# Performance work log

Measured on AMD Instinct MI355X. Metric: run time of the kernel, lower is better.

## Reference

```python
import jax, jax.numpy as jnp
import numpy as np

NUM_REC = 22
P = 24            # nodes per graph
G = 8192          # graphs in batch
N = G * P         # 196608 nodes
E = N * 4         # 786432 edges (avg degree 4)
F_NODE = 96       # 74 chem features + 22 receptor one-hot
F_EDGE = 16
EPS = 1e-5
NEG_SLOPE = 0.2   # GATv2 default negative_slope


def gatv2(x, src, dst, edge_attr, Wl, bl, Wr, br, We, att, bo):
    """PyG GATv2Conv (heads=1, add_self_loops=True, fill_value='mean'), eval mode."""
    n = x.shape[0]
    # self loops with edge_attr = mean of incoming edge attrs per target node
    deg = jax.ops.segment_sum(jnp.ones_like(dst, dtype=x.dtype), dst, num_segments=n)
    loop_attr = jax.ops.segment_sum(edge_attr, dst, num_segments=n) / jnp.maximum(deg, 1.0)[:, None]
    loop = jnp.arange(n, dtype=src.dtype)
    s = jnp.concatenate([src, loop])           # [E+N] source
    d = jnp.concatenate([dst, loop])           # [E+N] target
    ea = jnp.concatenate([edge_attr, loop_attr], axis=0)
    xl = x @ Wl + bl                           # source transform [n, C]
    xr = x @ Wr + br                           # target transform [n, C]
    m = xl[s] + xr[d] + ea @ We                # [E+N, C]
    e = jax.nn.leaky_relu(m, NEG_SLOPE) @ att  # [E+N] attention logits
    # segment softmax over target nodes (every node has its self loop -> no empty segment)
    emax = jax.ops.segment_max(e, d, num_segments=n)
    ez = jnp.exp(e - emax[d])
    denom = jax.ops.segment_sum(ez, d, num_segments=n)
    alpha = ez / denom[d]
    return jax.ops.segment_sum(alpha[:, None] * xl[s], d, num_segments=n) + bo


def batchnorm(h, gamma, beta):
    # training-style BN (batch statistics, biased var) as in torch BatchNorm1d forward
    mu = h.mean(0)
    var = h.var(0)
    return gamma * (h - mu) * jax.lax.rsqrt(var + EPS) + beta


def setup_inputs() -> dict:
    key = jax.random.key(0)
    ks = jax.random.split(key, 40)
    x = jax.random.normal(ks[0], (N, F_NODE), jnp.float32)
    # intra-graph, self-loop-free edges
    src = jax.random.randint(ks[1], (E,), 0, N)
    off = jax.random.randint(ks[2], (E,), 1, P)
    dst = (src // P) * P + (src % P + off) % P
    edge_index = jnp.stack([src, dst]).astype(jnp.int32)
    edge_attr = jax.random.normal(ks[3], (E, F_EDGE), jnp.float32)
    batch = (jnp.arange(N) // P).astype(jnp.int32)

    def lin(k, i, o):
        return jax.random.normal(k, (i, o), jnp.float32) * 0.1

    def vec(k, o):
        return jax.random.normal(k, (o,), jnp.float32) * 0.1

    Fin = F_NODE - NUM_REC  # 74
    return {
        "x": x, "edge_index": edge_index, "edge_attr": edge_attr, "batch": batch,
        # GATv2 layer 1 (74 -> 32)
        "Wl1": lin(ks[4], Fin, 32), "bl1": vec(ks[5], 32),
        "Wr1": lin(ks[6], Fin, 32), "br1": vec(ks[7], 32),
        "We1": lin(ks[8], F_EDGE, 32), "att1": vec(ks[9], 32), "bo1": vec(ks[10], 32),
        # GATv2 layer 2 (32 -> 8)
        "Wl2": lin(ks[11], 32, 8), "bl2": vec(ks[12], 8),
        "Wr2": lin(ks[13], 32, 8), "br2": vec(ks[14], 8),
        "We2": lin(ks[15], F_EDGE, 8), "att2": vec(ks[16], 8), "bo2": vec(ks[17], 8),
        # BatchNorm affine
        "g1": jnp.ones((32,), jnp.float32), "be1": jnp.zeros((32,), jnp.float32),
        "g2": jnp.ones((8,), jnp.float32), "be2": jnp.zeros((8,), jnp.float32),
        # MLP head (8+22=30 -> 32 -> 16 -> 8 -> 4 -> 2)
        "fc1_W": lin(ks[18], 8 + NUM_REC, 32), "fc1_b": vec(ks[19], 32),
        "fc2_W": lin(ks[20], 32, 16), "fc2_b": vec(ks[21], 16),
        "fc3_W": lin(ks[22], 16, 8), "fc3_b": vec(ks[23], 8),
        "fc4_W": lin(ks[24], 8, 4), "fc4_b": vec(ks[25], 4),
        "out_W": lin(ks[26], 4, 2), "out_b": vec(ks[27], 2),
    }


def reference(x, edge_index, edge_attr, batch,
              Wl1, bl1, Wr1, br1, We1, att1, bo1,
              Wl2, bl2, Wr2, br2, We2, att2, bo2,
              g1, be1, g2, be2,
              fc1_W, fc1_b, fc2_W, fc2_b, fc3_W, fc3_b, fc4_W, fc4_b, out_W, out_b):
    src, dst = edge_index[0], edge_index[1]
    # per-graph receptor features = last NUM_REC cols of the first node of each graph
    first_idx = jnp.searchsorted(batch, jnp.arange(G, dtype=batch.dtype))
    rec_feat = x[first_idx, -NUM_REC:]                       # [G, 22]
    xin = x[:, :-NUM_REC]                                    # [N, 74]

    h = jax.nn.relu(gatv2(xin, src, dst, edge_attr, Wl1, bl1, Wr1, br1, We1, att1, bo1))
    h = batchnorm(h, g1, be1)                                # [N, 32]
    h = jax.nn.sigmoid(gatv2(h, src, dst, edge_attr, Wl2, bl2, Wr2, br2, We2, att2, bo2))
    h = batchnorm(h, g2, be2)                                # [N, 8]

    cnt = jax.ops.segment_sum(jnp.ones((x.shape[0], 1), x.dtype), batch, num_segments=G)
    pooled = jax.ops.segment_sum(h, batch, num_segments=G) / cnt  # global_mean_pool [G, 8]

    z = jnp.concatenate([pooled, rec_feat], axis=1)          # [G, 30]
    z = jax.nn.relu(z @ fc1_W + fc1_b)
    z = jax.nn.relu(z @ fc2_W + fc2_b)
    z = jax.nn.relu(z @ fc3_W + fc3_b)
    z = jax.nn.relu(z @ fc4_W + fc4_b)
    return z @ out_W + out_b                                 # [G, 2]
```

## Files before the change

### kernel.cpp

```cpp
#include <hip/hip_runtime.h>

typedef unsigned short u16;
typedef unsigned int   u32;
typedef __attribute__((ext_vector_type(4))) float f4_t;
typedef __attribute__((ext_vector_type(4))) unsigned short us4_t;

#define GG 8192
#define PP 24
#define NN 196608
#define EE 786432
#define CAP 176

#define oWl1 0
#define oWr1 2368
#define obl1 4736
#define obr1 4768
#define oWe1 4800
#define oatt1 5312
#define obo1 5344
#define oWl2 5376
#define oWr2 5632
#define obl2 5888
#define obr2 5896
#define oWe2 5904
#define oatt2 6032
#define obo2 6040
#define ofc1W 6048
#define ofc1b 7008
#define ofc2W 7040
#define ofc2b 7552
#define ofc3W 7568
#define ofc3b 7696
#define ofc4W 7704
#define ofc4b 7736
#define ooutW 7740
#define ooutb 7748

#define oW1I 0
#define oW2P 4864
#define oB2P 5376

__device__ __forceinline__ float bf2f(u16 u){
  union { u32 i; float f; } x; x.i = ((u32)u) << 16; return x.f;
}
__device__ __forceinline__ u32 fkey(float f){
  int i = __float_as_int(f);
  return (i >= 0) ? (((u32)i) | 0x80000000u) : ~((u32)i);
}
__device__ __forceinline__ float funkey(u32 k){
  u32 i = (k & 0x80000000u) ? (k & 0x7FFFFFFFu) : ~k;
  return __uint_as_float(i);
}
__device__ __forceinline__ float lrelu(float m){ return m > 0.f ? m : 0.2f*m; }
__device__ __forceinline__ float sexp(float a){ return __expf(fminf(a, 0.f)); }
__device__ __forceinline__ float ldf(const void* p, size_t i, int isf){
  return isf ? ((const float*)p)[i] : bf2f(((const u16*)p)[i]);
}

__global__ void k_zero(float* __restrict__ out){
  int i = blockIdx.x*256 + threadIdx.x;
  if(i < GG*2) out[i] = 0.f;
}

__global__ void k_count(const int* __restrict__ dst, int* __restrict__ cnt){
  int e = blockIdx.x*256 + threadIdx.x;
  if(e < EE){
    u32 d = (u32)dst[e];
    if(d < (u32)NN) atomicAdd(&cnt[d], 1);
  }
}

__global__ void k_scanA(const int* __restrict__ cnt, int* __restrict__ offs,
                        int* __restrict__ bsum){
  __shared__ int part[1024];
  int t = threadIdx.x;
  int i = blockIdx.x*1024 + t;
  int c = cnt[i];
  part[t] = c; __syncthreads();
  for(int off=1; off<1024; off<<=1){
    int v = (t>=off) ? part[t-off] : 0;
    __syncthreads();
    part[t] += v;
    __syncthreads();
  }
  offs[i] = part[t] - c;
  if(t==1023) bsum[blockIdx.x] = part[1023];
}

__global__ void k_scanB(int* __restrict__ bsum, int* __restrict__ offs){
  __shared__ int part[256];
  int t = threadIdx.x;
  int c = (t < 192) ? bsum[t] : 0;
  part[t] = c; __syncthreads();
  for(int off=1; off<256; off<<=1){
    int v = (t>=off) ? part[t-off] : 0;
    __syncthreads();
    part[t] += v;
    __syncthreads();
  }
  if(t < 192) bsum[t] = part[t] - c;
  if(t == 255) offs[NN] = part[255];
}

__global__ void k_scanC(int* __restrict__ offs, const int* __restrict__ bsum,
                        int* __restrict__ cursor){
  int t = threadIdx.x;
  int i = blockIdx.x*1024 + t;
  int v = offs[i] + bsum[blockIdx.x];
  offs[i] = v;
  cursor[i] = v;
}

__global__ void k_scatter(const int* __restrict__ src, const int* __restrict__ dst,
                          int* __restrict__ cursor, int* __restrict__ spack){
  int e = blockIdx.x*256 + threadIdx.x;
  if(e < EE){
    u32 d = (u32)dst[e];
    if(d >= (u32)NN) return;
    int g = d / PP;
    int pos = atomicAdd(&cursor[d], 1);
    if((u32)pos < (u32)EE){
      int sl = src[e] - g*PP;
      if((u32)sl > 23u) sl = 0;
      spack[pos] = sl | ((int)(d - g*PP) << 5) | (e << 10);
    }
  }
}

__global__ void k_eaperm(const int* __restrict__ spack, const int* __restrict__ offs,
                         const void* __restrict__ ea, const int* __restrict__ dflag,
                         float* __restrict__ eap){
  int i = blockIdx.x*256 + threadIdx.x;
  if(i >= EE) return;
  if(i >= offs[NN]) return;
  int isf = dflag[0];
  u32 id = ((u32)spack[i]) >> 10;
  if(id >= (u32)EE) id = 0;
  float* o = eap + (size_t)i*16;
  if(isf){
    const float* er = (const float*)ea + (size_t)id*16;
    #pragma unroll
    for(int q=0;q<4;q++) *(f4_t*)(o + q*4) = *(const f4_t*)(er + q*4);
  } else {
    const u16* er = (const u16*)ea + (size_t)id*16;
    #pragma unroll
    for(int c=0;c<16;c++) o[c] = bf2f(er[c]);
  }
}

__global__ void k_wconv(float* __restrict__ wb, float* __restrict__ wq, int* __restrict__ dflag,
    const u32* __restrict__ xw,
    const void* Wl1, const void* bl1, const void* Wr1, const void* br1,
    const void* We1, const void* att1, const void* bo1,
    const void* Wl2, const void* bl2, const void* Wr2, const void* br2,
    const void* We2, const void* att2, const void* bo2,
    const void* f1W, const void* f1b, const void* f2W, const void* f2b,
    const void* f3W, const void* f3b, const void* f4W, const void* f4b,
    const void* oW,  const void* ob)
{
  __shared__ u32 mx[256];
  int t = threadIdx.x;
  u32 m = 0;
  for(int i=t; i<2048; i+=256){
    u32 e = (xw[i] >> 7) & 0xFFu;
    m = m > e ? m : e;
  }
  mx[t] = m; __syncthreads();
  for(int off=128; off>0; off>>=1){
    if(t<off) mx[t] = mx[t] > mx[t+off] ? mx[t] : mx[t+off];
    __syncthreads();
  }
  int isf = (mx[0] > 140u) ? 1 : 0;
  if(t==0) dflag[0] = isf;
  #define CP(off,src,len) for(int i=t;i<(len);i+=256) wb[(off)+i]=ldf(src,i,isf);
  CP(oWl1,Wl1,2368) CP(oWr1,Wr1,2368) CP(obl1,bl1,32) CP(obr1,br1,32)
  CP(oWe1,We1,512)  CP(oatt1,att1,32) CP(obo1,bo1,32)
  CP(oWl2,Wl2,256)  CP(oWr2,Wr2,256)  CP(obl2,bl2,8)  CP(obr2,br2,8)
  CP(oWe2,We2,128)  CP(oatt2,att2,8)  CP(obo2,bo2,8)
  CP(ofc1W,f1W,960) CP(ofc1b,f1b,32)  CP(ofc2W,f2W,512) CP(ofc2b,f2b,16)
  CP(ofc3W,f3W,128) CP(ofc3b,f3b,8)   CP(ofc4W,f4W,32)  CP(ofc4b,f4b,4)
  CP(ooutW,oW,8)    CP(ooutb,ob,2)
  #undef CP
  for(int i=t; i<76*64; i+=256){
    int k = i>>6, cc = i&63, mat = cc>>5, c = cc&31;
    wq[oW1I + i] = (k < 74) ? ldf(mat ? Wr1 : Wl1, k*32 + c, isf) : 0.f;
  }
}

__global__ void k_prep2(float* __restrict__ wq, const float* __restrict__ wb,
                        const float* __restrict__ stats1){
  int t = threadIdx.x;
  for(int i=t; i<512; i+=256){
    int k = i>>4, cc = i&15, mat = cc>>3, c = cc&7;
    wq[oW2P + i] = stats1[k] * wb[(mat ? oWr2 : oWl2) + k*8 + c];
  }
  if(t < 16){
    int mat = t>>3, c = t&7;
    float s = wb[(mat ? obr2 : obl2) + c];
    for(int k=0;k<32;k++) s += stats1[32+k] * wb[(mat ? oWr2 : oWl2) + k*8 + c];
    wq[oB2P + t] = s;
  }
}

__global__ __launch_bounds__(256, 6) void k_l1stats(
    const void* __restrict__ x, const void* __restrict__ ea, const float* __restrict__ eap,
    const float* __restrict__ wb, const float* __restrict__ wq,
    const int* __restrict__ offs, const int* __restrict__ spack, const int* __restrict__ dflag,
    float* __restrict__ p1sum, float* __restrict__ p1sq,
    float* __restrict__ h1, int use_h1)
{
  __shared__ __align__(16) float sEaF[CAP][16];
  __shared__ __align__(16) float sXl[24][36];
  __shared__ float sXr[24][33];
  __shared__ float sEaSum[24][17];
  __shared__ float sEv[CAP];
  __shared__ int   sSl[CAP];
  __shared__ int   sRO[25];
  __shared__ float sSelfE[24];
  __shared__ float sPS[4][32], sPQ[4][32];

  const int t = threadIdx.x;
  const int g = blockIdx.x;
  const int wid = t >> 6;
  const int lane = t & 63;
  const int isf = dflag[0];
  const int nb = g*PP;
  const int eb = offs[nb];
  int ecnt = offs[nb+24] - eb; if(ecnt < 0) ecnt = 0; if(ecnt > CAP) ecnt = CAP;

  if(t < 25){
    int v = offs[nb+t] - eb;
    if(v < 0) v = 0; if(v > CAP) v = CAP;
    sRO[t] = v;
  }
  if(eap){
    for(int i=t; i<ecnt; i+=256) sSl[i] = spack[eb+i] & 1023;
    for(int i=t; i<ecnt*4; i+=256){
      int e = i>>2, q = i&3;
      *(f4_t*)&sEaF[e][q*4] = *(const f4_t*)(eap + ((size_t)(eb+e))*16 + q*4);
    }
  } else {
    for(int i=t; i<ecnt; i+=256){
      int sp = spack[eb+i];
      sSl[i] = sp & 1023;
      u32 id = ((u32)sp) >> 10;
      if(id >= (u32)EE) id = 0;
      if(isf){
        const float* er = (const float*)ea + (size_t)id*16;
        #pragma unroll
        for(int q=0;q<4;q++) *(f4_t*)&sEaF[i][q*4] = *(const f4_t*)(er + q*4);
      } else {
        #pragma unroll
        for(int c=0;c<16;c++) sEaF[i][c] = bf2f(((const u16*)ea)[(size_t)id*16 + c]);
      }
    }
  }
  {
    int rz = wid*6;
    for(int i=lane; i<6*17; i+=64) sEaSum[rz + i/17][i%17] = 0.f;
  }

  {
    const int c = t & 31, mat = (t>>5)&1, w = wid, cc = t&63;
    const float* gW = wq + oW1I;
    float bi = wb[(mat ? obr1 : obl1) + c];
    float acc[6];
    #pragma unroll
    for(int j=0;j<6;j++) acc[j] = bi;
    if(isf){
      const float* xr0 = (const float*)x + (size_t)(nb + w*6)*96;
      for(int kb=0; kb<19; kb++){
        float w0 = gW[(kb*4+0)*64 + cc];
        float w1 = gW[(kb*4+1)*64 + cc];
        float w2 = gW[(kb*4+2)*64 + cc];
        float w3 = gW[(kb*4+3)*64 + cc];
        #pragma unroll
        for(int j=0;j<6;j++){
          f4_t xv = *(const f4_t*)(xr0 + (size_t)j*96 + kb*4);
          acc[j] += xv[0]*w0 + xv[1]*w1 + xv[2]*w2 + xv[3]*w3;
        }
      }
    } else {
      const u16* xr0 = (const u16*)x + (size_t)(nb + w*6)*96;
      for(int kb=0; kb<19; kb++){
        float w0 = gW[(kb*4+0)*64 + cc];
        float w1 = gW[(kb*4+1)*64 + cc];
        float w2 = gW[(kb*4+2)*64 + cc];
        float w3 = gW[(kb*4+3)*64 + cc];
        #pragma unroll
        for(int j=0;j<6;j++){
          us4_t xv = *(const us4_t*)(xr0 + (size_t)j*96 + kb*4);
          acc[j] += bf2f(xv[0])*w0 + bf2f(xv[1])*w1 + bf2f(xv[2])*w2 + bf2f(xv[3])*w3;
        }
      }
    }
    if(mat){
      #pragma unroll
      for(int j=0;j<6;j++) sXr[w*6+j][c] = acc[j];
    } else {
      #pragma unroll
      for(int j=0;j<6;j++) sXl[w*6+j][c] = acc[j];
    }
  }
  __syncthreads();

  const int r0 = wid*6;
  const int a0 = sRO[r0], a1 = sRO[r0+6];
  const int c = t & 31, eo = (t>>5)&1;

  float wr[16];
  #pragma unroll
  for(int k=0;k<16;k++) wr[k] = wb[oWe1 + k*32 + c];
  const float av = wb[oatt1 + c];
  const float bv = wb[obo1 + c];

  for(int base=a0; base<a1; base+=2){
    int e = base + eo;
    bool valid = (e < a1);
    int ec = valid ? e : a0;
    int sp = sSl[ec];
    int sl = sp & 31; if(sl > 23) sl = 0;
    int dl = (sp >> 5) & 31; if(dl > 23) dl = 0;
    f4_t A0 = *(const f4_t*)&sEaF[ec][0];
    f4_t A1 = *(const f4_t*)&sEaF[ec][4];
    f4_t A2 = *(const f4_t*)&sEaF[ec][8];
    f4_t A3 = *(const f4_t*)&sEaF[ec][12];
    float p = A0[0]*wr[0]+A0[1]*wr[1]+A0[2]*wr[2]+A0[3]*wr[3]
            + A1[0]*wr[4]+A1[1]*wr[5]+A1[2]*wr[6]+A1[3]*wr[7]
            + A2[0]*wr[8]+A2[1]*wr[9]+A2[2]*wr[10]+A2[3]*wr[11]
            + A3[0]*wr[12]+A3[1]*wr[13]+A3[2]*wr[14]+A3[3]*wr[15];
    if(valid && c < 16) atomicAdd(&sEaSum[dl][c], sEaF[ec][c]);
    float v = lrelu(sXl[sl][c] + sXr[dl][c] + p) * av;
    v += __shfl_xor(v, 16);
    v += __shfl_xor(v, 8);
    v += __shfl_xor(v, 4);
    v += __shfl_xor(v, 2);
    v += __shfl_xor(v, 1);
    if(valid && c == 0) sEv[e] = v;
  }

  #pragma unroll
  for(int rp=0; rp<3; rp++){
    int r = r0 + rp*2 + eo;
    int deg = sRO[r+1] - sRO[r];
    float invd = 1.f / (float)(deg > 0 ? deg : 1);
    float mp = 0.f;
    #pragma unroll
    for(int k=0;k<16;k++) mp += sEaSum[r][k] * wr[k];
    float v = lrelu(sXl[r][c] + sXr[r][c] + mp*invd) * av;
    v += __shfl_xor(v, 16);
    v += __shfl_xor(v, 8);
    v += __shfl_xor(v, 4);
    v += __shfl_xor(v, 2);
    v += __shfl_xor(v, 1);
    if(c == 0) sSelfE[r] = v;
  }

  float ps = 0.f, pq = 0.f;
  const int h = (t >> 5) & 1;
  #pragma unroll
  for(int j=0;j<6;j++){
    int r = r0 + j;
    int a = sRO[r], b = sRO[r+1];
    float selfE = sSelfE[r];
    float mx = -3.4e38f;
    for(int e=a+lane; e<b; e+=64) mx = fmaxf(mx, sEv[e]);
    mx = fmaxf(mx, __shfl_xor(mx, 32));
    mx = fmaxf(mx, __shfl_xor(mx, 16));
    mx = fmaxf(mx, __shfl_xor(mx, 8));
    mx = fmaxf(mx, __shfl_xor(mx, 4));
    mx = fmaxf(mx, __shfl_xor(mx, 2));
    mx = fmaxf(mx, __shfl_xor(mx, 1));
    float m = fmaxf(mx, selfE);
    float ds = 0.f;
    for(int e=a+lane; e<b; e+=64){
      float z = sexp(sEv[e] - m);
      sEv[e] = z;
      ds += z;
    }
    ds += __shfl_xor(ds, 32);
    ds += __shfl_xor(ds, 16);
    ds += __shfl_xor(ds, 8);
    ds += __shfl_xor(ds, 4);
    ds += __shfl_xor(ds, 2);
    ds += __shfl_xor(ds, 1);
    float selfZ = sexp(selfE - m);
    float rden = 1.f / fmaxf(ds + selfZ, 1e-30f);
    float acc = 0.f;
    for(int e=a+h; e<b; e+=2){
      int sl = sSl[e] & 31; if(sl > 23) sl = 0;
      acc += sEv[e] * sXl[sl][c];
    }
    acc += __shfl_xor(acc, 32);
    float out = (acc + selfZ * sXl[r][c]) * rden;
    out = fmaxf(out + bv, 0.f);
    if(h == 0){
      if(use_h1) h1[((size_t)nb + r)*32 + c] = out;
      ps += out; pq += out*out;
    }
  }
  if(h == 0){ sPS[wid][c] = ps; sPQ[wid][c] = pq; }
  __syncthreads();
  if(t < 32){
    p1sum[g*32+t] = sPS[0][t]+sPS[1][t]+sPS[2][t]+sPS[3][t];
    p1sq[g*32+t]  = sPQ[0][t]+sPQ[1][t]+sPQ[2][t]+sPQ[3][t];
  }
}

__global__ void k_reduce(const float* __restrict__ ps, const float* __restrict__ pq,
                         const void* __restrict__ gamma, const void* __restrict__ beta,
                         const int* __restrict__ dflag,
                         float* __restrict__ stats, int F){
  __shared__ float rs[256], rq[256];
  int f = blockIdx.x, t = threadIdx.x;
  float s=0.f, q=0.f;
  for(int g=t; g<GG; g+=256){ s += ps[g*F+f]; q += pq[g*F+f]; }
  rs[t]=s; rq[t]=q; __syncthreads();
  for(int off=128; off>0; off>>=1){
    if(t<off){ rs[t]+=rs[t+off]; rq[t]+=rq[t+off]; }
    __syncthreads();
  }
  if(t==0){
    int isf = dflag[0];
    float mu  = rs[0] * (1.f/(float)NN);
    float var = rq[0] * (1.f/(float)NN) - mu*mu;
    if(var < 0.f) var = 0.f;
    float sc  = ldf(gamma,f,isf) / sqrtf(var + 1e-5f);
    stats[f]   = sc;
    stats[F+f] = ldf(beta,f,isf) - mu*sc;
  }
}

__global__ __launch_bounds__(256, 6) void k_fused2_h1(
    const void* __restrict__ ea, const float* __restrict__ eap,
    const float* __restrict__ wb, const float* __restrict__ wq,
    const float* __restrict__ h1,
    const int* __restrict__ offs, const int* __restrict__ spack, const int* __restrict__ dflag,
    float* __restrict__ gsum2, float* __restrict__ gsq2)
{
  __shared__ __align__(16) float sEaF[CAP][16];
  __shared__ float sXl2[24][12], sXr2[24][12];
  __shared__ float sEaSum[24][17];
  __shared__ float sEv[CAP];
  __shared__ int   sSl[CAP];
  __shared__ int   sRO[25];
  __shared__ float sSelfE[24];
  __shared__ float sGS[4][8], sGQ[4][8];

  const int t = threadIdx.x;
  const int g = blockIdx.x;
  const int wid = t >> 6;
  const int lane = t & 63;
  const int isf = dflag[0];
  const int nb = g*PP;
  const int eb = offs[nb];
  int ecnt = offs[nb+24] - eb; if(ecnt < 0) ecnt = 0; if(ecnt > CAP) ecnt = CAP;

  if(t < 25){
    int v = offs[nb+t] - eb;
    if(v < 0) v = 0; if(v > CAP) v = CAP;
    sRO[t] = v;
  }
  if(eap){
    for(int i=t; i<ecnt; i+=256) sSl[i] = spack[eb+i] & 1023;
    for(int i=t; i<ecnt*4; i+=256){
      int e = i>>2, q = i&3;
      *(f4_t*)&sEaF[e][q*4] = *(const f4_t*)(eap + ((size_t)(eb+e))*16 + q*4);
    }
  } else {
    for(int i=t; i<ecnt; i+=256){
      int sp = spack[eb+i];
      sSl[i] = sp & 1023;
      u32 id = ((u32)sp) >> 10;
      if(id >= (u32)EE) id = 0;
      if(isf){
        const float* er = (const float*)ea + (size_t)id*16;
        #pragma unroll
        for(int q=0;q<4;q++) *(f4_t*)&sEaF[i][q*4] = *(const f4_t*)(er + q*4);
      } else {
        #pragma unroll
        for(int c=0;c<16;c++) sEaF[i][c] = bf2f(((const u16*)ea)[(size_t)id*16 + c]);
      }
    }
  }
  {
    int rz = wid*6;
    for(int i=lane; i<6*17; i+=64) sEaSum[rz + i/17][i%17] = 0.f;
    for(int i=lane; i<96; i+=64){
      int rl = i>>4, cc = i&15;
      int r = rz + rl;
      float s = wq[oB2P + cc];
      const float* hr = h1 + ((size_t)nb + r)*32;
      #pragma unroll
      for(int q=0;q<8;q++){
        f4_t hv = *(const f4_t*)(hr + q*4);
        s += hv[0]*wq[oW2P+(q*4+0)*16+cc] + hv[1]*wq[oW2P+(q*4+1)*16+cc]
           + hv[2]*wq[oW2P+(q*4+2)*16+cc] + hv[3]*wq[oW2P+(q*4+3)*16+cc];
      }
      if(cc < 8) sXl2[r][cc] = s; else sXr2[r][cc-8] = s;
    }
  }
  __syncthreads();

  const int r0 = wid*6;
  const int a0 = sRO[r0], a1 = sRO[r0+6];
  const int c = t & 7;
  const int eo = lane >> 3;

  float wr[16];
  #pragma unroll
  for(int k=0;k<16;k++) wr[k] = wb[oWe2 + k*8 + c];
  const float av = wb[oatt2 + c];
  const float bv = wb[obo2 + c];

  for(int base=a0; base<a1; base+=8){
    int e = base + eo;
    bool valid = (e < a1);
    int ec = valid ? e : a0;
    int sp = sSl[ec];
    int sl = sp & 31; if(sl > 23) sl = 0;
    int dl = (sp >> 5) & 31; if(dl > 23) dl = 0;
    f4_t A0 = *(const f4_t*)&sEaF[ec][0];
    f4_t A1 = *(const f4_t*)&sEaF[ec][4];
    f4_t A2 = *(const f4_t*)&sEaF[ec][8];
    f4_t A3 = *(const f4_t*)&sEaF[ec][12];
    float p = A0[0]*wr[0]+A0[1]*wr[1]+A0[2]*wr[2]+A0[3]*wr[3]
            + A1[0]*wr[4]+A1[1]*wr[5]+A1[2]*wr[6]+A1[3]*wr[7]
            + A2[0]*wr[8]+A2[1]*wr[9]+A2[2]*wr[10]+A2[3]*wr[11]
            + A3[0]*wr[12]+A3[1]*wr[13]+A3[2]*wr[14]+A3[3]*wr[15];
    if(valid){
      atomicAdd(&sEaSum[dl][c],   sEaF[ec][c]);
      atomicAdd(&sEaSum[dl][c+8], sEaF[ec][c+8]);
    }
    float v = lrelu(sXl2[sl][c] + sXr2[dl][c] + p) * av;
    v += __shfl_xor(v, 4);
    v += __shfl_xor(v, 2);
    v += __shfl_xor(v, 1);
    if(valid && c == 0) sEv[e] = v;
  }

  {
    int rr = r0 + (eo < 6 ? eo : 0);
    bool valid = (eo < 6);
    int deg = sRO[rr+1] - sRO[rr];
    float invd = 1.f / (float)(deg > 0 ? deg : 1);
    float mp = 0.f;
    #pragma unroll
    for(int k=0;k<16;k++) mp += sEaSum[rr][k] * wr[k];
    float v = lrelu(sXl2[rr][c] + sXr2[rr][c] + mp*invd) * av;
    v += __shfl_xor(v, 4);
    v += __shfl_xor(v, 2);
    v += __shfl_xor(v, 1);
    if(valid && c == 0) sSelfE[rr] = v;
  }

  float gs = 0.f, gq = 0.f;
  #pragma unroll
  for(int j=0;j<6;j++){
    int r = r0 + j;
    int a = sRO[r], b = sRO[r+1];
    float selfE = sSelfE[r];
    float mx = -3.4e38f;
    for(int e=a+lane; e<b; e+=64) mx = fmaxf(mx, sEv[e]);
    mx = fmaxf(mx, __shfl_xor(mx, 32));
    mx = fmaxf(mx, __shfl_xor(mx, 16));
    mx = fmaxf(mx, __shfl_xor(mx, 8));
    mx = fmaxf(mx, __shfl_xor(mx, 4));
    mx = fmaxf(mx, __shfl_xor(mx, 2));
    mx = fmaxf(mx, __shfl_xor(mx, 1));
    float m = fmaxf(mx, selfE);
    float ds = 0.f;
    for(int e=a+lane; e<b; e+=64){
      float z = sexp(sEv[e] - m);
      sEv[e] = z;
      ds += z;
    }
    ds += __shfl_xor(ds, 32);
    ds += __shfl_xor(ds, 16);
    ds += __shfl_xor(ds, 8);
    ds += __shfl_xor(ds, 4);
    ds += __shfl_xor(ds, 2);
    ds += __shfl_xor(ds, 1);
    float selfZ = sexp(selfE - m);
    float rden = 1.f / fmaxf(ds + selfZ, 1e-30f);
    float acc = 0.f;
    for(int e=a+eo; e<b; e+=8){
      int sl = sSl[e] & 31; if(sl > 23) sl = 0;
      acc += sEv[e] * sXl2[sl][c];
    }
    acc += __shfl_xor(acc, 8);
    acc += __shfl_xor(acc, 16);
    acc += __shfl_xor(acc, 32);
    float out = (acc + selfZ * sXl2[r][c]) * rden;
    float s = 1.f / (1.f + __expf(-(out + bv)));
    if(eo == 0){ gs += s; gq += s*s; }
  }
  if(eo == 0){ sGS[wid][c] = gs; sGQ[wid][c] = gq; }
  __syncthreads();
  if(t < 8){
    gsum2[g*8+t] = sGS[0][t]+sGS[1][t]+sGS[2][t]+sGS[3][t];
    gsq2[g*8+t]  = sGQ[0][t]+sGQ[1][t]+sGQ[2][t]+sGQ[3][t];
  }
}

__global__ __launch_bounds__(256) void k_fused2_rec(
    const void* __restrict__ x, const void* __restrict__ ea,
    const float* __restrict__ wb, const float* __restrict__ stats1,
    const int* __restrict__ offs, const int* __restrict__ spack, const int* __restrict__ dflag,
    float* __restrict__ gsum2, float* __restrict__ gsq2)
{
  __shared__ float sXrow[24][76];
  __shared__ float sEaF[CAP][17];
  __shared__ __align__(16) float sXl[24][36];
  __shared__ __align__(16) float sXr[24][36];
  __shared__ __align__(16) float sOut[24][36];
  __shared__ float sH[24][33];
  __shared__ float sXl2[24][12], sXr2[24][12], sOut2[24][12];
  __shared__ float sEapSum[24][32];
  __shared__ float sEv[CAP], sEz[CAP];
  __shared__ int   sSp[CAP];
  __shared__ int   sDeg[24];
  __shared__ u32   sMaxU[24];
  __shared__ float sMaxF[24], sDen[24], sSelfZ[24];
  __shared__ float sAtt[32], sBo[32], sSc[32], sSh[32];

  const int t = threadIdx.x;
  const int g = blockIdx.x;
  const int isf = dflag[0];
  int eb = offs[g*24], ee = offs[(g+1)*24];
  if(eb < 0) eb = 0; if(eb > EE) eb = EE;
  if(ee < eb) ee = eb; if(ee > EE) ee = EE;
  int ecnt = ee - eb; if(ecnt > CAP) ecnt = CAP;

  for(int i=t; i<24*74; i+=256){
    int r = i/74, c = i%74;
    sXrow[r][c] = ldf(x, (size_t)(g*PP + r)*96 + c, isf);
  }
  for(int i=t; i<CAP; i+=256) sSp[i] = (i<ecnt) ? spack[eb+i] : 0;
  if(t < 32){ sAtt[t]=wb[oatt1+t]; sBo[t]=wb[obo1+t]; sSc[t]=stats1[t]; sSh[t]=stats1[32+t]; }
  if(t < 24){ sDeg[t]=0; sMaxU[t]=0u; sDen[t]=0.f; }
  for(int i=t; i<24*32; i+=256) sEapSum[i>>5][i&31] = 0.f;
  __syncthreads();
  for(int i=t; i<CAP*16; i+=256){
    int e = i>>4, c = i&15;
    float v = 0.f;
    if(e < ecnt){
      u32 id = ((u32)sSp[e]) >> 10;
      if(id >= (u32)EE) id = 0;
      v = ldf(ea, (size_t)id*16 + c, isf);
    }
    sEaF[e][c] = v;
  }
  __syncthreads();

  {
    int c = t & 31, rr0 = t >> 5;
    for(int r = rr0; r < 24; r += 8){
      float al = wb[obl1+c], ar = wb[obr1+c];
      for(int k=0;k<74;k++){
        float xv = sXrow[r][k];
        al += xv * wb[oWl1 + k*32 + c];
        ar += xv * wb[oWr1 + k*32 + c];
      }
      sXl[r][c] = al; sXr[r][c] = ar;
    }
  }
  __syncthreads();

  for(int e=t; e<ecnt; e+=256){
    int sp = sSp[e];
    int sl = sp & 31; if(sl > 23) sl = 0;
    int dl = (sp >> 5) & 31; if(dl > 23) dl = 0;
    float ev = 0.f;
    for(int c=0;c<32;c++){
      float p = 0.f;
      for(int k=0;k<16;k++) p += sEaF[e][k] * wb[oWe1 + k*32 + c];
      atomicAdd(&sEapSum[dl][c], p);
      ev += lrelu(sXl[sl][c] + sXr[dl][c] + p) * sAtt[c];
    }
    sEv[e] = ev;
    atomicMax(&sMaxU[dl], fkey(ev));
    atomicAdd(&sDeg[dl], 1);
  }
  __syncthreads();

  if(t < 24){
    float invd = 1.f / (float)(sDeg[t] > 0 ? sDeg[t] : 1);
    float ev = 0.f;
    for(int c=0;c<32;c++)
      ev += lrelu(sXl[t][c] + sXr[t][c] + sEapSum[t][c]*invd) * sAtt[c];
    float mxv = (sDeg[t] > 0) ? fmaxf(funkey(sMaxU[t]), ev) : ev;
    sMaxF[t] = mxv;
    float z = sexp(ev - mxv);
    sSelfZ[t] = z;
    sDen[t] = z;
  }
  __syncthreads();

  for(int e=t; e<ecnt; e+=256){
    int dl = (sSp[e]>>5)&31; if(dl > 23) dl = 0;
    float z = sexp(sEv[e] - sMaxF[dl]);
    sEz[e] = z;
    atomicAdd(&sDen[dl], z);
  }
  __syncthreads();

  for(int e=t; e<ecnt; e+=256){
    int dl = (sSp[e]>>5)&31; if(dl > 23) dl = 0;
    sEz[e] /= fmaxf(sDen[dl], 1e-30f);
  }
  if(t < 24) sSelfZ[t] /= fmaxf(sDen[t], 1e-30f);
  __syncthreads();

  for(int o=t; o<24*8; o+=256){
    int nl = o >> 3, cq = (o & 7)*4;
    float al = sSelfZ[nl];
    f4_t xv = *(const f4_t*)&sXl[nl][cq];
    f4_t r;
    #pragma unroll
    for(int j=0;j<4;j++) r[j] = al*xv[j];
    *(f4_t*)&sOut[nl][cq] = r;
  }
  __syncthreads();

  for(int o=t; o<ecnt*8; o+=256){
    int e = o >> 3, cq = (o & 7)*4;
    int sp = sSp[e];
    int sl = sp & 31; if(sl > 23) sl = 0;
    int dl = (sp >> 5) & 31; if(dl > 23) dl = 0;
    float al = sEz[e];
    f4_t xv = *(const f4_t*)&sXl[sl][cq];
    atomicAdd(&sOut[dl][cq+0], al*xv[0]);
    atomicAdd(&sOut[dl][cq+1], al*xv[1]);
    atomicAdd(&sOut[dl][cq+2], al*xv[2]);
    atomicAdd(&sOut[dl][cq+3], al*xv[3]);
  }
  __syncthreads();

  for(int i=t; i<24*32; i+=256){
    int r = i>>5, c = i&31;
    float v = fmaxf(sOut[r][c] + sBo[c], 0.f);
    sH[r][c] = v*sSc[c] + sSh[c];
  }
  __syncthreads();
  if(t < 24){ sDeg[t]=0; sMaxU[t]=0u; sDen[t]=0.f; }
  for(int i=t; i<24*8; i+=256) sEapSum[i>>3][i&7] = 0.f;
  __syncthreads();

  if(t < 24*8*2){
    int mat = t/192, rem = t%192, r = rem/8, c = rem&7;
    const float* Wm = wb + (mat ? oWr2 : oWl2);
    float s = wb[(mat ? obr2 : obl2) + c];
    for(int k=0;k<32;k++) s += sH[r][k]*Wm[k*8+c];
    if(mat) sXr2[r][c] = s; else sXl2[r][c] = s;
  }
  __syncthreads();

  for(int e=t; e<ecnt; e+=256){
    int sp = sSp[e];
    int sl = sp & 31; if(sl > 23) sl = 0;
    int dl = (sp >> 5) & 31; if(dl > 23) dl = 0;
    float ev = 0.f;
    for(int c=0;c<8;c++){
      float p = 0.f;
      for(int k=0;k<16;k++) p += sEaF[e][k] * wb[oWe2 + k*8 + c];
      atomicAdd(&sEapSum[dl][c], p);
      ev += lrelu(sXl2[sl][c] + sXr2[dl][c] + p) * wb[oatt2+c];
    }
    sEv[e] = ev;
    atomicMax(&sMaxU[dl], fkey(ev));
    atomicAdd(&sDeg[dl], 1);
  }
  __syncthreads();

  if(t < 24){
    float invd = 1.f / (float)(sDeg[t] > 0 ? sDeg[t] : 1);
    float ev = 0.f;
    for(int c=0;c<8;c++)
      ev += lrelu(sXl2[t][c] + sXr2[t][c] + sEapSum[t][c]*invd) * wb[oatt2+c];
    float mxv = (sDeg[t] > 0) ? fmaxf(funkey(sMaxU[t]), ev) : ev;
    sMaxF[t] = mxv;
    float z = sexp(ev - mxv);
    sSelfZ[t] = z;
    sDen[t] = z;
  }
  __syncthreads();

  for(int e=t; e<ecnt; e+=256){
    int dl = (sSp[e]>>5)&31; if(dl > 23) dl = 0;
    float z = sexp(sEv[e] - sMaxF[dl]);
    sEz[e] = z;
    atomicAdd(&sDen[dl], z);
  }
  __syncthreads();

  for(int e=t; e<ecnt; e+=256){
    int dl = (sSp[e]>>5)&31; if(dl > 23) dl = 0;
    sEz[e] /= fmaxf(sDen[dl], 1e-30f);
  }
  if(t < 24) sSelfZ[t] /= fmaxf(sDen[t], 1e-30f);
  __syncthreads();

  for(int o=t; o<24*8; o+=256){
    int nl = o >> 3, c = o & 7;
    sOut2[nl][c] = sSelfZ[nl] * sXl2[nl][c];
  }
  __syncthreads();

  for(int o=t; o<ecnt*8; o+=256){
    int e = o >> 3, c = o & 7;
    int sp = sSp[e];
    int sl = sp & 31; if(sl > 23) sl = 0;
    int dl = (sp >> 5) & 31; if(dl > 23) dl = 0;
    atomicAdd(&sOut2[dl][c], sEz[e]*sXl2[sl][c]);
  }
  __syncthreads();

  if(t < 8){
    float gs=0.f, gq=0.f;
    for(int nl=0; nl<24; nl++){
      float v = sOut2[nl][t] + wb[obo2+t];
      float s = 1.f / (1.f + __expf(-v));
      gs += s; gq += s*s;
    }
    gsum2[g*8+t] = gs; gsq2[g*8+t] = gq;
  }
}

__global__ __launch_bounds__(256) void k_mlp(
    const float* __restrict__ gsum2, const float* __restrict__ stats2,
    const void* __restrict__ x, const int* __restrict__ dflag,
    const float* __restrict__ wb, float* __restrict__ out)
{
  __shared__ float w[1702];
  int t = threadIdx.x;
  for(int i=t; i<1702; i+=256) w[i] = wb[6048+i];
  __syncthreads();
  int g = blockIdx.x*256 + t;
  int isf = dflag[0];
  float a[30], b[32];
  for(int c=0;c<8;c++) a[c] = stats2[c]*(gsum2[(size_t)g*8+c]*(1.f/24.f)) + stats2[8+c];
  size_t xoff = (size_t)g*PP*96 + 74;
  for(int j=0;j<22;j++) a[8+j] = ldf(x, xoff+j, isf);
  for(int o=0;o<32;o++){ float s = w[960+o];  for(int i=0;i<30;i++) s += a[i]*w[i*32+o];      b[o]=fmaxf(s,0.f); }
  for(int o=0;o<16;o++){ float s = w[1504+o]; for(int i=0;i<32;i++) s += b[i]*w[992+i*16+o];  a[o]=fmaxf(s,0.f); }
  for(int o=0;o<8;o++){  float s = w[1648+o]; for(int i=0;i<16;i++) s += a[i]*w[1520+i*8+o];  b[o]=fmaxf(s,0.f); }
  for(int o=0;o<4;o++){  float s = w[1688+o]; for(int i=0;i<8;i++)  s += b[i]*w[1656+i*4+o];  a[o]=fmaxf(s,0.f); }
  for(int o=0;o<2;o++){
    float s = w[1700+o];
    for(int i=0;i<4;i++) s += a[i]*w[1692+i*2+o];
    out[(size_t)g*2+o] = s;
  }
}

extern "C" void kernel_launch(void* const* d_in, const int* in_sizes, int n_in,
                              void* d_out, int out_size, void* d_ws, size_t ws_size,
                              hipStream_t stream)
{
  (void)in_sizes; (void)n_in; (void)out_size;
  const void* x    = d_in[0];
  const int* eidx  = (const int*)d_in[1];
  const void* ea   = d_in[2];

  const int* srcA = eidx;
  const int* dstA = eidx + EE;

  constexpr size_t O_WB    = 0;
  constexpr size_t O_WQ    = 32768;
  constexpr size_t O_OFFS  = 57344;
  constexpr size_t O_CUR   = O_OFFS + (size_t)(NN+512)*4;
  constexpr size_t O_SPACK = O_CUR  + (size_t)NN*4;
  constexpr size_t O_P1S   = O_SPACK + (size_t)EE*4;
  constexpr size_t O_P1Q   = O_P1S   + (size_t)GG*32*4;
  constexpr size_t O_ST1   = O_P1Q   + (size_t)GG*32*4;
  constexpr size_t O_GS2   = O_ST1   + 256;
  constexpr size_t O_GQ2   = O_GS2   + (size_t)GG*8*4;
  constexpr size_t O_ST2   = O_GQ2   + (size_t)GG*8*4;
  constexpr size_t O_FLAG  = O_ST2   + 256;
  constexpr size_t REQUIRED_BASE = O_FLAG + 256;
  constexpr size_t O_H1    = REQUIRED_BASE;
  constexpr size_t REQUIRED_BIG = O_H1 + (size_t)NN*32*4;
  constexpr size_t O_EAP   = REQUIRED_BIG;
  constexpr size_t REQUIRED_EAP = O_EAP + (size_t)EE*16*4;

  if(ws_size < REQUIRED_BASE){
    k_zero<<<(GG*2+255)/256, 256, 0, stream>>>((float*)d_out);
    return;
  }
  const int use_h1  = (ws_size >= REQUIRED_BIG) ? 1 : 0;
  const int use_eap = (ws_size >= REQUIRED_EAP) ? 1 : 0;

  char* W = (char*)d_ws;
  float* wb     = (float*)(W + O_WB);
  float* wq     = (float*)(W + O_WQ);
  int*   offs   = (int*)(W + O_OFFS);
  int*   bsum   = offs + NN + 64;
  int*   cnt    = (int*)(W + O_CUR);
  int*   cursor = (int*)(W + O_CUR);
  int*   spack  = (int*)(W + O_SPACK);
  float* p1sum  = (float*)(W + O_P1S);
  float* p1sq   = (float*)(W + O_P1Q);
  float* stats1 = (float*)(W + O_ST1);
  float* gsum2  = (float*)(W + O_GS2);
  float* gsq2   = (float*)(W + O_GQ2);
  float* stats2 = (float*)(W + O_ST2);
  int*   dflag  = (int*)(W + O_FLAG);
  float* h1     = (float*)(W + O_H1);
  float* eap    = (float*)(W + O_EAP);

  hipMemsetAsync(cnt, 0, (size_t)NN*sizeof(int), stream);
  k_count  <<<EE/256, 256, 0, stream>>>(dstA, cnt);
  k_scanA  <<<192, 1024, 0, stream>>>(cnt, offs, bsum);
  k_scanB  <<<1, 256, 0, stream>>>(bsum, offs);
  k_scanC  <<<192, 1024, 0, stream>>>(offs, bsum, cursor);
  k_scatter<<<EE/256, 256, 0, stream>>>(srcA, dstA, cursor, spack);
  k_wconv  <<<1, 256, 0, stream>>>(wb, wq, dflag, (const u32*)x,
            d_in[4], d_in[5], d_in[6], d_in[7], d_in[8], d_in[9], d_in[10],
            d_in[11], d_in[12], d_in[13], d_in[14], d_in[15], d_in[16], d_in[17],
            d_in[22], d_in[23], d_in[24], d_in[25], d_in[26], d_in[27],
            d_in[28], d_in[29], d_in[30], d_in[31]);
  if(use_eap)
    k_eaperm<<<EE/256, 256, 0, stream>>>(spack, offs, ea, dflag, eap);
  k_l1stats<<<GG, 256, 0, stream>>>(x, ea, use_eap ? eap : (float*)nullptr,
                                    wb, wq, offs, spack, dflag,
                                    p1sum, p1sq, h1, use_h1);
  k_reduce <<<32, 256, 0, stream>>>(p1sum, p1sq, d_in[18], d_in[19], dflag, stats1, 32);
  k_prep2  <<<1, 256, 0, stream>>>(wq, wb, stats1);
  if(use_h1)
    k_fused2_h1 <<<GG, 256, 0, stream>>>(ea, use_eap ? eap : (float*)nullptr,
                                         wb, wq, h1, offs, spack, dflag, gsum2, gsq2);
  else
    k_fused2_rec<<<GG, 256, 0, stream>>>(x, ea, wb, stats1, offs, spack, dflag, gsum2, gsq2);
  k_reduce <<<8, 256, 0, stream>>>(gsum2, gsq2, d_in[20], d_in[21], dflag, stats2, 8);
  k_mlp    <<<GG/256, 256, 0, stream>>>(gsum2, stats2, x, dflag, wb, (float*)d_out);
}
```

Measured before the change: 705.3 us.

## Precompute per-edge edge_attr projections for both GAT layers in permute kernel

The edge-permutation kernel now multiplies each edge's attributes by We1 and We2 and stores the 32- and 8-wide projections in CSR order. New layer-1 and layer-2 kernels read these projections directly, and they build the self-loop mean term from the projected values by linearity instead of recomputing ea@We per edge. This removes the per-edge matmul from the fused graph kernels. In exchange, the permute kernel writes 160 bytes per edge instead of 64, so the layers read more memory, and the path needs a larger workspace.

Result: faster. 686.4 us (-2.7%).

```diff
diff --git a/kernel.cpp b/kernel.cpp
--- a/kernel.cpp
+++ b/kernel.cpp
@@ -148,6 +148,52 @@
   }
 }
 
+__global__ void k_eapermP(const int* __restrict__ spack, const int* __restrict__ offs,
+                          const void* __restrict__ ea, const int* __restrict__ dflag,
+                          const float* __restrict__ wb,
+                          float* __restrict__ p1, float* __restrict__ p2){
+  int i = blockIdx.x*256 + threadIdx.x;
+  if(i >= EE) return;
+  if(i >= offs[NN]) return;
+  int isf = dflag[0];
+  u32 id = ((u32)spack[i]) >> 10;
+  if(id >= (u32)EE) id = 0;
+  float eav[16];
+  if(isf){
+    const float* er = (const float*)ea + (size_t)id*16;
+    #pragma unroll
+    for(int k=0;k<16;k++) eav[k] = er[k];
+  } else {
+    const u16* er = (const u16*)ea + (size_t)id*16;
+    #pragma unroll
+    for(int k=0;k<16;k++) eav[k] = bf2f(er[k]);
+  }
+  float* o1 = p1 + (size_t)i*32;
+  #pragma unroll
+  for(int c=0;c<32;c+=4){
+    float s0=0.f, s1=0.f, s2=0.f, s3=0.f;
+    #pragma unroll
+    for(int k=0;k<16;k++){
+      f4_t w = *(const f4_t*)(wb + oWe1 + k*32 + c);
+      s0 += eav[k]*w[0]; s1 += eav[k]*w[1]; s2 += eav[k]*w[2]; s3 += eav[k]*w[3];
+    }
+    f4_t r; r[0]=s0; r[1]=s1; r[2]=s2; r[3]=s3;
+    *(f4_t*)(o1 + c) = r;
+  }
+  float* o2 = p2 + (size_t)i*8;
+  #pragma unroll
+  for(int c=0;c<8;c+=4){
+    float s0=0.f, s1=0.f, s2=0.f, s3=0.f;
+    #pragma unroll
+    for(int k=0;k<16;k++){
+      f4_t w = *(const f4_t*)(wb + oWe2 + k*8 + c);
+      s0 += eav[k]*w[0]; s1 += eav[k]*w[1]; s2 += eav[k]*w[2]; s3 += eav[k]*w[3];
+    }
+    f4_t r; r[0]=s0; r[1]=s1; r[2]=s2; r[3]=s3;
+    *(f4_t*)(o2 + c) = r;
+  }
+}
+
 __global__ void k_wconv(float* __restrict__ wb, float* __restrict__ wq, int* __restrict__ dflag,
     const u32* __restrict__ xw,
     const void* Wl1, const void* bl1, const void* Wr1, const void* br1,
@@ -199,6 +245,281 @@
     float s = wb[(mat ? obr2 : obl2) + c];
     for(int k=0;k<32;k++) s += stats1[32+k] * wb[(mat ? oWr2 : oWl2) + k*8 + c];
     wq[oB2P + t] = s;
+  }
+}
+
+__global__ __launch_bounds__(256, 6) void k_l1stats_p(
+    const void* __restrict__ x, const float* __restrict__ p1,
+    const float* __restrict__ wb, const float* __restrict__ wq,
+    const int* __restrict__ offs, const int* __restrict__ spack, const int* __restrict__ dflag,
+    float* __restrict__ p1sum, float* __restrict__ p1sq,
+    float* __restrict__ h1)
+{
+  __shared__ __align__(16) float sXl[24][36];
+  __shared__ __align__(16) float sXr[24][36];
+  __shared__ __align__(16) float sPS[24][32];
+  __shared__ __align__(16) float sPQ[24][32];
+  __shared__ float sEv[CAP];
+  __shared__ int   sSl[CAP];
+  __shared__ int   sRO[25];
+
+  const int t = threadIdx.x;
+  const int g = blockIdx.x;
+  const int isf = dflag[0];
+  const int nb = g*PP;
+  const int eb = offs[nb];
+  int ecnt = offs[nb+24] - eb;
+  if(ecnt < 0) ecnt = 0; if(ecnt > CAP) ecnt = CAP;
+
+  if(t < 25){
+    int v = offs[nb+t] - eb;
+    if(v < 0) v = 0; if(v > CAP) v = CAP;
+    sRO[t] = v;
+  }
+  for(int i=t; i<ecnt; i+=256){
+    int sl = spack[eb+i] & 31; if(sl > 23) sl = 0;
+    sSl[i] = sl;
+  }
+
+  {
+    const int c = t & 31, mat = (t>>5)&1, w = t>>6, cc = t&63;
+    const float* gW = wq + oW1I;
+    float bi = wb[(mat ? obr1 : obl1) + c];
+    float acc[6];
+    #pragma unroll
+    for(int j=0;j<6;j++) acc[j] = bi;
+    if(isf){
+      const float* xr0 = (const float*)x + (size_t)(nb + w*6)*96;
+      for(int kb=0; kb<19; kb++){
+        float w0 = gW[(kb*4+0)*64 + cc];
+        float w1 = gW[(kb*4+1)*64 + cc];
+        float w2 = gW[(kb*4+2)*64 + cc];
+        float w3 = gW[(kb*4+3)*64 + cc];
+        #pragma unroll
+        for(int j=0;j<6;j++){
+          f4_t xv = *(const f4_t*)(xr0 + (size_t)j*96 + kb*4);
+          acc[j] += xv[0]*w0 + xv[1]*w1 + xv[2]*w2 + xv[3]*w3;
+        }
+      }
+    } else {
+      const u16* xr0 = (const u16*)x + (size_t)(nb + w*6)*96;
+      for(int kb=0; kb<19; kb++){
+        float w0 = gW[(kb*4+0)*64 + cc];
+        float w1 = gW[(kb*4+1)*64 + cc];
+        float w2 = gW[(kb*4+2)*64 + cc];
+        float w3 = gW[(kb*4+3)*64 + cc];
+        #pragma unroll
+        for(int j=0;j<6;j++){
+          us4_t xv = *(const us4_t*)(xr0 + (size_t)j*96 + kb*4);
+          acc[j] += bf2f(xv[0])*w0 + bf2f(xv[1])*w1 + bf2f(xv[2])*w2 + bf2f(xv[3])*w3;
+        }
+      }
+    }
+    if(mat){
+      #pragma unroll
+      for(int j=0;j<6;j++) sXr[w*6+j][c] = acc[j];
+    } else {
+      #pragma unroll
+      for(int j=0;j<6;j++) sXl[w*6+j][c] = acc[j];
+    }
+  }
+  __syncthreads();
+
+  if(t < 192){
+    const int r = t >> 3, sub = t & 7;
+    const int a = sRO[r], b = sRO[r+1];
+    const int deg = b - a;
+    const float* att = wb + oatt1;
+
+    float emax = -3.4e38f;
+    for(int e=a+sub; e<b; e+=8){
+      int sl = sSl[e];
+      const float* pe = p1 + (size_t)(eb+e)*32;
+      float ev = 0.f;
+      #pragma unroll
+      for(int q=0;q<8;q++){
+        f4_t pv  = *(const f4_t*)(pe + q*4);
+        f4_t xlv = *(const f4_t*)&sXl[sl][q*4];
+        f4_t xrv = *(const f4_t*)&sXr[r][q*4];
+        ev += att[q*4+0]*lrelu(xlv[0]+xrv[0]+pv[0]);
+        ev += att[q*4+1]*lrelu(xlv[1]+xrv[1]+pv[1]);
+        ev += att[q*4+2]*lrelu(xlv[2]+xrv[2]+pv[2]);
+        ev += att[q*4+3]*lrelu(xlv[3]+xrv[3]+pv[3]);
+      }
+      sEv[e] = ev;
+      emax = fmaxf(emax, ev);
+    }
+    emax = fmaxf(emax, __shfl_xor(emax, 1));
+    emax = fmaxf(emax, __shfl_xor(emax, 2));
+    emax = fmaxf(emax, __shfl_xor(emax, 4));
+
+    float m0=0.f, m1=0.f, m2=0.f, m3=0.f;
+    for(int e=a; e<b; ++e){
+      f4_t pv = *(const f4_t*)(p1 + (size_t)(eb+e)*32 + sub*4);
+      m0 += pv[0]; m1 += pv[1]; m2 += pv[2]; m3 += pv[3];
+    }
+    float invd = 1.f / (float)(deg > 0 ? deg : 1);
+    float sv;
+    {
+      int c0 = sub*4;
+      sv  = att[c0+0]*lrelu(sXl[r][c0+0] + sXr[r][c0+0] + m0*invd);
+      sv += att[c0+1]*lrelu(sXl[r][c0+1] + sXr[r][c0+1] + m1*invd);
+      sv += att[c0+2]*lrelu(sXl[r][c0+2] + sXr[r][c0+2] + m2*invd);
+      sv += att[c0+3]*lrelu(sXl[r][c0+3] + sXr[r][c0+3] + m3*invd);
+    }
+    sv += __shfl_xor(sv, 1);
+    sv += __shfl_xor(sv, 2);
+    sv += __shfl_xor(sv, 4);
+
+    float m = fmaxf(emax, sv);
+    float ssum = 0.f;
+    for(int e=a+sub; e<b; e+=8){
+      float z = sexp(sEv[e] - m);
+      sEv[e] = z;
+      ssum += z;
+    }
+    ssum += __shfl_xor(ssum, 1);
+    ssum += __shfl_xor(ssum, 2);
+    ssum += __shfl_xor(ssum, 4);
+    float selfZ = sexp(sv - m);
+    float rden = 1.f / fmaxf(ssum + selfZ, 1e-30f);
+
+    float a0=0.f, a1=0.f, a2=0.f, a3=0.f;
+    for(int e=a; e<b; ++e){
+      float z = sEv[e];
+      f4_t xlv = *(const f4_t*)&sXl[sSl[e]][sub*4];
+      a0 += z*xlv[0]; a1 += z*xlv[1]; a2 += z*xlv[2]; a3 += z*xlv[3];
+    }
+    f4_t xself = *(const f4_t*)&sXl[r][sub*4];
+    f4_t outv, sqv;
+    {
+      float o;
+      o = (a0 + selfZ*xself[0]) * rden; o = fmaxf(o + wb[obo1+sub*4+0], 0.f); outv[0]=o; sqv[0]=o*o;
+      o = (a1 + selfZ*xself[1]) * rden; o = fmaxf(o + wb[obo1+sub*4+1], 0.f); outv[1]=o; sqv[1]=o*o;
+      o = (a2 + selfZ*xself[2]) * rden; o = fmaxf(o + wb[obo1+sub*4+2], 0.f); outv[2]=o; sqv[2]=o*o;
+      o = (a3 + selfZ*xself[3]) * rden; o = fmaxf(o + wb[obo1+sub*4+3], 0.f); outv[3]=o; sqv[3]=o*o;
+    }
+    *(f4_t*)&h1[((size_t)nb + r)*32 + sub*4] = outv;
+    *(f4_t*)&sPS[r][sub*4] = outv;
+    *(f4_t*)&sPQ[r][sub*4] = sqv;
+  }
+  __syncthreads();
+  if(t < 32){
+    float s=0.f, q=0.f;
+    #pragma unroll
+    for(int r=0;r<24;r++){ s += sPS[r][t]; q += sPQ[r][t]; }
+    p1sum[g*32+t] = s; p1sq[g*32+t] = q;
+  }
+}
+
+__global__ __launch_bounds__(256, 6) void k_fused2_p(
+    const float* __restrict__ p2,
+    const float* __restrict__ wb, const float* __restrict__ wq,
+    const float* __restrict__ h1,
+    const int* __restrict__ offs, const int* __restrict__ spack,
+    float* __restrict__ gsum2, float* __restrict__ gsq2)
+{
+  __shared__ float sXl2[24][13];
+  __shared__ float sXr2[24][13];
+  __shared__ float sEv[CAP];
+  __shared__ int   sSl[CAP];
+  __shared__ int   sRO[25];
+  __shared__ float sGS[24][8];
+  __shared__ float sGQ[24][8];
+
+  const int t = threadIdx.x;
+  const int g = blockIdx.x;
+  const int wid = t >> 6;
+  const int lane = t & 63;
+  const int nb = g*PP;
+  const int eb = offs[nb];
+  int ecnt = offs[nb+24] - eb;
+  if(ecnt < 0) ecnt = 0; if(ecnt > CAP) ecnt = CAP;
+
+  if(t < 25){
+    int v = offs[nb+t] - eb;
+    if(v < 0) v = 0; if(v > CAP) v = CAP;
+    sRO[t] = v;
+  }
+  for(int i=t; i<ecnt; i+=256){
+    int sl = spack[eb+i] & 31; if(sl > 23) sl = 0;
+    sSl[i] = sl;
+  }
+  {
+    int rz = wid*6;
+    for(int i=lane; i<96; i+=64){
+      int rl = i>>4, cc = i&15;
+      int r = rz + rl;
+      float s = wq[oB2P + cc];
+      const float* hr = h1 + ((size_t)nb + r)*32;
+      #pragma unroll
+      for(int q=0;q<8;q++){
+        f4_t hv = *(const f4_t*)(hr + q*4);
+        s += hv[0]*wq[oW2P+(q*4+0)*16+cc] + hv[1]*wq[oW2P+(q*4+1)*16+cc]
+           + hv[2]*wq[oW2P+(q*4+2)*16+cc] + hv[3]*wq[oW2P+(q*4+3)*16+cc];
+      }
+      if(cc < 8) sXl2[r][cc] = s; else sXr2[r][cc-8] = s;
+    }
+  }
+  __syncthreads();
+
+  if(t < 192){
+    const int r = t >> 3, sub = t & 7;
+    const int a = sRO[r], b = sRO[r+1];
+    const int deg = b - a;
+    const float* att2 = wb + oatt2;
+
+    float emax = -3.4e38f;
+    for(int e=a+sub; e<b; e+=8){
+      int sl = sSl[e];
+      const float* pe = p2 + (size_t)(eb+e)*8;
+      float ev = 0.f;
+      #pragma unroll
+      for(int j=0;j<8;j++)
+        ev += att2[j]*lrelu(sXl2[sl][j] + sXr2[r][j] + pe[j]);
+      sEv[e] = ev;
+      emax = fmaxf(emax, ev);
+    }
+    emax = fmaxf(emax, __shfl_xor(emax, 1));
+    emax = fmaxf(emax, __shfl_xor(emax, 2));
+    emax = fmaxf(emax, __shfl_xor(emax, 4));
+
+    float mpc = 0.f;
+    for(int e=a; e<b; ++e)
+      mpc += p2[(size_t)(eb+e)*8 + sub];
+    float invd = 1.f / (float)(deg > 0 ? deg : 1);
+    float sv = att2[sub]*lrelu(sXl2[r][sub] + sXr2[r][sub] + mpc*invd);
+    sv += __shfl_xor(sv, 1);
+    sv += __shfl_xor(sv, 2);
+    sv += __shfl_xor(sv, 4);
+
+    float m = fmaxf(emax, sv);
+    float ssum = 0.f;
+    for(int e=a+sub; e<b; e+=8){
+      float z = sexp(sEv[e] - m);
+      sEv[e] = z;
+      ssum += z;
+    }
+    ssum += __shfl_xor(ssum, 1);
+    ssum += __shfl_xor(ssum, 2);
+    ssum += __shfl_xor(ssum, 4);
+    float selfZ = sexp(sv - m);
+    float rden = 1.f / fmaxf(ssum + selfZ, 1e-30f);
+
+    float acc = 0.f;
+    for(int e=a; e<b; ++e)
+      acc += sEv[e] * sXl2[sSl[e]][sub];
+    float o = (acc + selfZ*sXl2[r][sub]) * rden;
+    float s = 1.f / (1.f + __expf(-(o + wb[obo2+sub])));
+    sGS[r][sub] = s;
+    sGQ[r][sub] = s*s;
+  }
+  __syncthreads();
+  if(t < 8){
+    float gs=0.f, gq=0.f;
+    #pragma unroll
+    for(int r=0;r<24;r++){ gs += sGS[r][t]; gq += sGQ[r][t]; }
+    gsum2[g*8+t] = gs; gsq2[g*8+t] = gq;
   }
 }
 
@@ -880,15 +1201,18 @@
   constexpr size_t REQUIRED_BASE = O_FLAG + 256;
   constexpr size_t O_H1    = REQUIRED_BASE;
   constexpr size_t REQUIRED_BIG = O_H1 + (size_t)NN*32*4;
-  constexpr size_t O_EAP   = REQUIRED_BIG;
-  constexpr size_t REQUIRED_EAP = O_EAP + (size_t)EE*16*4;
+  constexpr size_t O_EAP1  = REQUIRED_BIG;
+  constexpr size_t O_EAP2  = O_EAP1 + (size_t)EE*32*4;
+  constexpr size_t REQUIRED_P = O_EAP2 + (size_t)EE*8*4;
+  constexpr size_t REQUIRED_EAP16 = O_EAP1 + (size_t)EE*16*4;
 
   if(ws_size < REQUIRED_BASE){
     k_zero<<<(GG*2+255)/256, 256, 0, stream>>>((float*)d_out);
     return;
   }
-  const int use_h1  = (ws_size >= REQUIRED_BIG) ? 1 : 0;
-  const int use_eap = (ws_size >= REQUIRED_EAP) ? 1 : 0;
+  const int use_h1  = (ws_size >= REQUIRED_BIG)   ? 1 : 0;
+  const int use_p   = (ws_size >= REQUIRED_P)     ? 1 : 0;
+  const int use_eap = (!use_p && ws_size >= REQUIRED_EAP16) ? 1 : 0;
 
   char* W = (char*)d_ws;
   float* wb     = (float*)(W + O_WB);
@@ -906,7 +1230,8 @@
   float* stats2 = (float*)(W + O_ST2);
   int*   dflag  = (int*)(W + O_FLAG);
   float* h1     = (float*)(W + O_H1);
-  float* eap    = (float*)(W + O_EAP);
+  float* eap1   = (float*)(W + O_EAP1);
+  float* eap2   = (float*)(W + O_EAP2);
 
   hipMemsetAsync(cnt, 0, (size_t)NN*sizeof(int), stream);
   k_count  <<<EE/256, 256, 0, stream>>>(dstA, cnt);
@@ -919,16 +1244,24 @@
             d_in[11], d_in[12], d_in[13], d_in[14], d_in[15], d_in[16], d_in[17],
             d_in[22], d_in[23], d_in[24], d_in[25], d_in[26], d_in[27],
             d_in[28], d_in[29], d_in[30], d_in[31]);
-  if(use_eap)
-    k_eaperm<<<EE/256, 256, 0, stream>>>(spack, offs, ea, dflag, eap);
-  k_l1stats<<<GG, 256, 0, stream>>>(x, ea, use_eap ? eap : (float*)nullptr,
-                                    wb, wq, offs, spack, dflag,
-                                    p1sum, p1sq, h1, use_h1);
+  if(use_p){
+    k_eapermP<<<EE/256, 256, 0, stream>>>(spack, offs, ea, dflag, wb, eap1, eap2);
+    k_l1stats_p<<<GG, 256, 0, stream>>>(x, eap1, wb, wq, offs, spack, dflag,
+                                        p1sum, p1sq, h1);
+  } else {
+    if(use_eap)
+      k_eaperm<<<EE/256, 256, 0, stream>>>(spack, offs, ea, dflag, eap1);
+    k_l1stats<<<GG, 256, 0, stream>>>(x, ea, use_eap ? eap1 : (float*)nullptr,
+                                      wb, wq, offs, spack, dflag,
+                                      p1sum, p1sq, h1, use_h1);
+  }
   k_reduce <<<32, 256, 0, stream>>>(p1sum, p1sq, d_in[18], d_in[19], dflag, stats1, 32);
   k_prep2  <<<1, 256, 0, stream>>>(wq, wb, stats1);
-  if(use_h1)
-    k_fused2_h1 <<<GG, 256, 0, stream>>>(ea, use_eap ? eap : (float*)nullptr,
-                                         wb, wq, h1, offs, spack, dflag, gsum2, gsq2);
+  if(use_p)
+    k_fused2_p<<<GG, 256, 0, stream>>>(eap2, wb, wq, h1, offs, spack, gsum2, gsq2);
+  else if(use_h1)
+    k_fused2_h1<<<GG, 256, 0, stream>>>(ea, use_eap ? eap1 : (float*)nullptr,
+                                        wb, wq, h1, offs, spack, dflag, gsum2, gsq2);
   else
     k_fused2_rec<<<GG, 256, 0, stream>>>(x, ea, wb, stats1, offs, spack, dflag, gsum2, gsq2);
   k_reduce <<<8, 256, 0, stream>>>(gsum2, gsq2, d_in[20], d_in[21], dflag, stats2, 8);
```
